# Kernel optimization log

Hardware: AMD Instinct MI355X
Metric: run time of the kernel (lower is better)

## Reference

```python
import jax, jax.numpy as jnp
import numpy as np
from math import comb

N, D, ORDER, P = 32768, 8, 19, 20
O = ORDER + 1


def bernstein(X, order):
    # X: [N, D] in [0,1] -> Bernstein basis [N, D, order+1]
    o = order + 1
    r = jnp.arange(o, dtype=X.dtype)
    binom = jnp.asarray([comb(order, k) for k in range(o)], dtype=X.dtype)
    Xe = X[..., None]
    return (Xe ** r) * ((1.0 - Xe) ** (order - r)) * binom


def setup_inputs() -> dict:
    key = jax.random.key(0)
    k0, k1, k2, k3, k4, k5 = jax.random.split(key, 6)
    X = jax.random.uniform(k0, (N, D), dtype=jnp.float32)
    # perm: each row is a permutation of range(D) (as in the module default)
    perm = jax.vmap(lambda k: jax.random.permutation(k, D))(jax.random.split(k1, P)).astype(jnp.int32)
    meanw0 = -0.2 + 0.1 * jax.random.normal(k2, (P, 1, O), dtype=jnp.float32)
    meanw = -0.2 + 0.1 * jax.random.normal(k3, (D - 1, P, O, O), dtype=jnp.float32)
    varw0 = 0.05 * jax.random.normal(k4, (P, 1, O), dtype=jnp.float32)
    varw = 0.05 * jax.random.normal(k5, (D - 1, P, O, O), dtype=jnp.float32)
    return {"X": X, "perm": perm, "meanw0": meanw0, "meanw": meanw,
            "varw0": varw0, "varw": varw}


def reference(X, perm, meanw0, meanw, varw0, varw):
    outB = bernstein(X, ORDER)                       # [N, D, O]
    outBp = jnp.transpose(outB[:, perm], (1, 0, 2, 3))  # gather axis=1 -> [P, N, D, O]

    # ---- f_mean: chain of small matmuls with exp(meanw_i), gated by basis ----
    f = jnp.exp(meanw0) * outBp[:, :, 0, :]          # [P,1,O]*[P,N,O] -> [P,N,O]
    for i in range(1, D):
        f = jnp.einsum('pno,poq->pnq', f, jnp.exp(meanw[i - 1])) * outBp[:, :, i, :]
    mean = jnp.sum(jnp.sum(f, axis=-1), axis=0)[:, None]   # [N,1]

    # ---- f_var: six moment chains one..six, exp(meanw)^2 * exp(varw)^k ----
    kk = jnp.arange(1, 7, dtype=X.dtype).reshape(6, 1, 1, 1)
    B2_0 = outBp[:, :, 0, :] ** 2                    # [P,N,O]
    acc = jnp.exp(2.0 * meanw0 + kk * varw0) * B2_0[None]  # [6,P,N,O]
    for i in range(1, D):
        Wi = jnp.exp(2.0 * meanw[i - 1] + kk * varw[i - 1])  # [6,P,O,O]
        acc = jnp.einsum('kpno,kpoq->kpnq', acc, Wi) * (outBp[:, :, i, :] ** 2)[None]
    mom = jnp.sum(acc, axis=-1)                      # [6,P,N]
    c = jnp.asarray([1.0, 1 / 2, 1 / 6, 1 / 24, 1 / 120, 1 / 720], dtype=X.dtype)
    var = jnp.einsum('k,kpn->n', c, mom)[:, None]    # [N,1]

    return jnp.concatenate([mean, var], axis=-1)     # [N,2]
```

## Files before the change

kernel.cpp:

```cpp
#include <hip/hip_runtime.h>
#include <math.h>

#define NPTS 32768
#define DD 8
#define OO 20
#define PP 20
#define NCHAIN 7
#define NT 2

typedef _Float16 half8 __attribute__((ext_vector_type(8)));
typedef __fp16 fp16x2 __attribute__((ext_vector_type(2)));
typedef float floatx16 __attribute__((ext_vector_type(16)));
typedef unsigned int u32;

#define AS1 __attribute__((address_space(1)))
#define AS3 __attribute__((address_space(3)))

__device__ __forceinline__ int sigma_row(int m) {
    return (m >= 4 && m < 12) ? (m ^ 12) : m;
}

__device__ __forceinline__ void basis20(float tv, float* g) {
    constexpr float binom[OO] = {
        1.f, 19.f, 171.f, 969.f, 3876.f, 11628.f, 27132.f, 50388.f, 75582.f,
        92378.f, 92378.f, 75582.f, 50388.f, 27132.f, 11628.f, 3876.f, 969.f,
        171.f, 19.f, 1.f};
    float a = tv, b = 1.f - tv, v = 1.f;
#pragma unroll
    for (int q = 0; q < OO; ++q) { g[q] = v; v *= a; }
    v = 1.f;
#pragma unroll
    for (int q = OO - 1; q >= 0; --q) { g[q] = g[q] * v * binom[q]; v *= b; }
}

__device__ __forceinline__ unsigned pk2rtn(float a, float b) {
    union { _Float16 h[2]; unsigned u; } cv;
    cv.h[0] = (_Float16)a; cv.h[1] = (_Float16)b;
    return cv.u;
}

__device__ __forceinline__ unsigned pack_pk(float x, float y) {
    union { fp16x2 h; unsigned u; } cv;
    cv.h = __builtin_amdgcn_cvt_pkrtz(x, y);
    return cv.u;
}

__device__ __forceinline__ fp16x2 u2h(unsigned u) {
    union { unsigned u; fp16x2 h; } c; c.u = u; return c.h;
}
__device__ __forceinline__ unsigned h2u(fp16x2 h) {
    union { unsigned u; fp16x2 h; } c; c.h = h; return c.u;
}

__global__ void prep_kernel(const float* __restrict__ X,
                            const float* __restrict__ meanw0,
                            const float* __restrict__ meanw,
                            const float* __restrict__ varw0,
                            const float* __restrict__ varw,
                            float* __restrict__ W0,
                            _Float16* __restrict__ WA,
                            unsigned* __restrict__ G) {
    int e = blockIdx.x * 256 + threadIdx.x;
    const int n0 = NCHAIN * PP * OO;
    const int nW = NCHAIN * (DD - 1) * PP * 32 * 32;
    const int nG = NPTS * DD;
    if (e < n0) {
        int q = e % OO;
        int rem = e / OO;
        int p = rem % PP;
        int c = rem / PP;
        float m = meanw0[p * OO + q];
        W0[e] = (c == 0) ? __expf(m) : __expf(2.f * m + (float)c * varw0[p * OO + q]);
    } else if (e < n0 + nW) {
        int idx = e - n0;
        int j = idx & 7; idx >>= 3;
        int l = idx & 63; idx >>= 6;
        int f = idx & 1; idx >>= 1;
        int p = idx % PP; idx /= PP;
        int i = idx % (DD - 1);
        int c = idx / (DD - 1);
        int m = l & 31;
        int k = (l >> 5) * 8 + f * 16 + j;
        int q = sigma_row(m);
        float v = 0.f;
        if (q < OO && k < OO) {
            int mi = ((i * PP + p) * OO + k) * OO + q;
            float mm = meanw[mi];
            v = (c == 0) ? __expf(mm) : __expf(2.f * mm + (float)c * varw[mi]);
        }
        WA[e - n0] = (_Float16)v;
    } else if (e < n0 + nW + nG) {
        int idx = e - n0 - nW;
        int n = idx & (NPTS - 1);
        int d = idx >> 15;
        float g[OO];
        basis20(X[(size_t)n * DD + d], g);
        uint4 o0, o1, o2;
        o0.x = pk2rtn(g[0], g[1]);
        o0.y = pk2rtn(g[2], g[3]);
        o0.z = pk2rtn(g[4], g[5]);
        o0.w = pk2rtn(g[6], g[7]);
        o1.x = pk2rtn(g[16], g[17]);
        o1.y = pk2rtn(g[18], g[19]);
        o1.z = pk2rtn(g[8], g[9]);
        o1.w = pk2rtn(g[10], g[11]);
        o2.x = pk2rtn(g[12], g[13]);
        o2.y = pk2rtn(g[14], g[15]);
        o2.z = 0u;
        o2.w = 0u;
        uint4* out = (uint4*)(G + (size_t)(d * NPTS + n) * 12);
        out[0] = o0; out[1] = o1; out[2] = o2;
    }
}

__global__ __launch_bounds__(256, 2) void chain_kernel(
    const int* __restrict__ perm,
    const float* __restrict__ W0, const _Float16* __restrict__ WA,
    const unsigned* __restrict__ G, float* __restrict__ partial) {
    const int lane = threadIdx.x & 63;
    const int wv = threadIdx.x >> 6;
    const int nl = lane & 31;
    const bool hi = (lane >> 5) != 0;
    const int n0 = (blockIdx.x * 4 + wv) * (32 * NT);
    const int p = blockIdx.y;
    const int goffd = hi ? 6 : 0;

    __shared__ __align__(16) _Float16 Alds[2][NCHAIN * 1024];

    int dp[DD];
#pragma unroll
    for (int i = 0; i < DD; ++i) dp[i] = perm[p * DD + i];

    const unsigned uz = ((unsigned)dp[0]) >> 20;
    const float fz = __uint_as_float(uz);
    floatx16 kZero;
#pragma unroll
    for (int r = 0; r < 16; ++r) kZero[r] = fz;

    {
        const _Float16* wbase = WA + (size_t)p * 1024;
#pragma unroll
        for (int u = wv; u < 2 * NCHAIN; u += 4) {
            int c = u >> 1, h = u & 1;
            const _Float16* src =
                wbase + (size_t)c * (DD - 1) * PP * 1024 + h * 512 + lane * 8;
            __builtin_amdgcn_global_load_lds(
                (const AS1 u32*)src, (AS3 u32*)&Alds[0][u * 512], 16, 0, 0);
        }
    }

    unsigned st[NT][NCHAIN][6];

#pragma unroll
    for (int tile = 0; tile < NT; ++tile) {
        const uint2* rp = (const uint2*)(
            G + ((size_t)dp[0] * NPTS + (n0 + tile * 32 + nl)) * 12 + goffd);
        uint2 r0 = rp[0], r1 = rp[1], r2 = rp[2];
        unsigned gw[6] = {r0.x, r0.y, r1.x, r1.y, r2.x, r2.y};
        float gcf[12], scf[12];
#pragma unroll
        for (int q = 0; q < 6; ++q) {
            fp16x2 gh = u2h(gw[q]);
            gcf[2 * q] = (float)gh.x; gcf[2 * q + 1] = (float)gh.y;
        }
#pragma unroll
        for (int r = 0; r < 12; ++r) scf[r] = gcf[r] * gcf[r];
#pragma unroll
        for (int c = 0; c < NCHAIN; ++c) {
            const float* w0r = W0 + (c * PP + p) * OO;
            float val[12];
#pragma unroll
            for (int r = 0; r < 8; ++r) {
                float ws = hi ? w0r[r + 8] : w0r[r];
                val[r] = ws * (c == 0 ? gcf[r] : scf[r]);
            }
#pragma unroll
            for (int r = 8; r < 12; ++r) {
                float ws = hi ? 0.f : w0r[r + 8];
                val[r] = ws * (c == 0 ? gcf[r] : scf[r]);
            }
#pragma unroll
            for (int e = 0; e < 6; ++e)
                st[tile][c][e] = pack_pk(val[2 * e], val[2 * e + 1]);
        }
    }

    const float coef[NCHAIN] = {0.f, 1.f, 0.5f, 1.f / 6.f, 1.f / 24.f,
                                1.f / 120.f, 1.f / 720.f};
    float sm[NT], sv[NT];
#pragma unroll
    for (int tile = 0; tile < NT; ++tile) { sm[tile] = 0.f; sv[tile] = 0.f; }

    __syncthreads();

#pragma unroll
    for (int i = 1; i < DD; ++i) {
        const int cur = (i - 1) & 1;

        if (i < DD - 1) {
            const _Float16* wbase = WA + (size_t)(i * PP + p) * 1024;
#pragma unroll
            for (int u = wv; u < 2 * NCHAIN; u += 4) {
                int c = u >> 1, h = u & 1;
                const _Float16* src =
                    wbase + (size_t)c * (DD - 1) * PP * 1024 + h * 512 + lane * 8;
                __builtin_amdgcn_global_load_lds(
                    (const AS1 u32*)src, (AS3 u32*)&Alds[cur ^ 1][u * 512], 16, 0, 0);
            }
        }

        unsigned gw[NT][6], sw[NT][6];
#pragma unroll
        for (int tile = 0; tile < NT; ++tile) {
            const uint2* rp = (const uint2*)(
                G + ((size_t)dp[i] * NPTS + (n0 + tile * 32 + nl)) * 12 + goffd);
            uint2 r0 = rp[0], r1 = rp[1], r2 = rp[2];
            gw[tile][0] = r0.x; gw[tile][1] = r0.y;
            gw[tile][2] = r1.x; gw[tile][3] = r1.y;
            gw[tile][4] = r2.x; gw[tile][5] = r2.y;
        }
        if (i < DD - 1) {
#pragma unroll
            for (int tile = 0; tile < NT; ++tile)
#pragma unroll
                for (int e = 0; e < 6; ++e) {
                    fp16x2 gh = u2h(gw[tile][e]);
                    sw[tile][e] = h2u(gh * gh);
                }
        }

        float gcf[NT][12], scf[NT][12];
        if (i == DD - 1) {
#pragma unroll
            for (int tile = 0; tile < NT; ++tile) {
#pragma unroll
                for (int q = 0; q < 6; ++q) {
                    fp16x2 gh = u2h(gw[tile][q]);
                    gcf[tile][2 * q] = (float)gh.x; gcf[tile][2 * q + 1] = (float)gh.y;
                }
#pragma unroll
                for (int r = 0; r < 12; ++r)
                    scf[tile][r] = gcf[tile][r] * gcf[tile][r];
            }
        }

#pragma unroll
        for (int c = 0; c < NCHAIN; ++c) {
            const _Float16* ab = &Alds[cur][c * 1024 + lane * 8];
            half8 A0 = *(const half8*)(ab);
            half8 A1 = *(const half8*)(ab + 512);

#pragma unroll
            for (int tile = 0; tile < NT; ++tile) {
                union { unsigned u[4]; half8 h; } B0, B1;
                B0.u[0] = st[tile][c][0]; B0.u[1] = st[tile][c][1];
                B0.u[2] = st[tile][c][2]; B0.u[3] = st[tile][c][3];
                B1.u[0] = st[tile][c][4]; B1.u[1] = st[tile][c][5];
                B1.u[2] = uz;             B1.u[3] = uz;

                floatx16 acc;
                acc = __builtin_amdgcn_mfma_f32_32x32x16_f16(A0, B0.h, kZero, 0, 0, 0);
                acc = __builtin_amdgcn_mfma_f32_32x32x16_f16(A1, B1.h, acc, 0, 0, 0);

                if (i < DD - 1) {
#pragma unroll
                    for (int e = 0; e < 6; ++e) {
                        fp16x2 pr = __builtin_amdgcn_cvt_pkrtz(acc[2 * e], acc[2 * e + 1]);
                        fp16x2 gv = u2h(c == 0 ? gw[tile][e] : sw[tile][e]);
                        st[tile][c][e] = h2u(pr * gv);
                    }
                } else {
                    float s = 0.f;
#pragma unroll
                    for (int r = 0; r < 12; ++r)
                        s += acc[r] * (c == 0 ? gcf[tile][r] : scf[tile][r]);
                    if (c == 0) sm[tile] = s;
                    else        sv[tile] += coef[c] * s;
                }
            }
        }

        if (i < DD - 1) __syncthreads();
    }

#pragma unroll
    for (int tile = 0; tile < NT; ++tile) {
        float m = sm[tile] + __shfl_xor(sm[tile], 32, 64);
        float v = sv[tile] + __shfl_xor(sv[tile], 32, 64);
        if (lane < 32) {
            partial[(size_t)p * NPTS + n0 + tile * 32 + nl] = m;
            partial[(size_t)(PP + p) * NPTS + n0 + tile * 32 + nl] = v;
        }
    }
}

__global__ void reduce_kernel(const float* __restrict__ partial,
                              float* __restrict__ out) {
    int n = blockIdx.x * 256 + threadIdx.x;
    float m = 0.f, v = 0.f;
#pragma unroll
    for (int p = 0; p < PP; ++p) {
        m += partial[(size_t)p * NPTS + n];
        v += partial[(size_t)(PP + p) * NPTS + n];
    }
    out[2 * n] = m;
    out[2 * n + 1] = v;
}

extern "C" void kernel_launch(void* const* d_in, const int* in_sizes, int n_in,
                              void* d_out, int out_size, void* d_ws, size_t ws_size,
                              hipStream_t stream) {
    const float* X      = (const float*)d_in[0];
    const int*   perm   = (const int*)d_in[1];
    const float* meanw0 = (const float*)d_in[2];
    const float* meanw  = (const float*)d_in[3];
    const float* varw0  = (const float*)d_in[4];
    const float* varw   = (const float*)d_in[5];
    float* out = (float*)d_out;

    float*     W0      = (float*)d_ws;
    _Float16*  WA      = (_Float16*)((char*)d_ws + 11200);
    unsigned*  G       = (unsigned*)((char*)d_ws + 11200 + 2007040);
    float*     partial = (float*)((char*)d_ws + 11200 + 2007040 + 12582912);

    int prep_n = NCHAIN * PP * OO + NCHAIN * (DD - 1) * PP * 32 * 32 + NPTS * DD;
    hipLaunchKernelGGL(prep_kernel, dim3((prep_n + 255) / 256), dim3(256), 0,
                       stream, X, meanw0, meanw, varw0, varw, W0, WA, G);

    dim3 grid(NPTS / (128 * NT), PP);
    hipLaunchKernelGGL(chain_kernel, grid, dim3(256), 0, stream,
                       perm, W0, WA, G, partial);

    hipLaunchKernelGGL(reduce_kernel, dim3(NPTS / 256), dim3(256), 0, stream,
                       partial, out);
}
```

Measured before the change: 145.2 us.

## Fuse final reduction into chain kernel via atomic counter; shrink basis stride

The separate reduce kernel is replaced by a last-block-done pattern: each chain block bumps a per-column atomic counter and the block that finishes last sums the P partials and writes the output. This removes one kernel launch and its dependency gap. The basis table G is also packed at 10 words per point instead of 12, dropping the zero padding, and the padded lanes are filled with zero in registers. This cuts G storage and load traffic, at the cost of a fence, an atomic and a serialized reduction tail inside the chain kernel.

```diff
diff --git a/kernel.cpp b/kernel.cpp
--- a/kernel.cpp
+++ b/kernel.cpp
@@ -7,6 +7,7 @@
 #define PP 20
 #define NCHAIN 7
 #define NT 2
+#define GSTRIDE 10
 
 typedef _Float16 half8 __attribute__((ext_vector_type(8)));
 typedef __fp16 fp16x2 __attribute__((ext_vector_type(2)));
@@ -59,7 +60,8 @@
                             const float* __restrict__ varw,
                             float* __restrict__ W0,
                             _Float16* __restrict__ WA,
-                            unsigned* __restrict__ G) {
+                            unsigned* __restrict__ G,
+                            unsigned* __restrict__ cnt) {
     int e = blockIdx.x * 256 + threadIdx.x;
     const int n0 = NCHAIN * PP * OO;
     const int nW = NCHAIN * (DD - 1) * PP * 32 * 32;
@@ -95,28 +97,29 @@
         int d = idx >> 15;
         float g[OO];
         basis20(X[(size_t)n * DD + d], g);
-        uint4 o0, o1, o2;
+        uint2 o0, o1, o2, o3, o4;
         o0.x = pk2rtn(g[0], g[1]);
         o0.y = pk2rtn(g[2], g[3]);
-        o0.z = pk2rtn(g[4], g[5]);
-        o0.w = pk2rtn(g[6], g[7]);
-        o1.x = pk2rtn(g[16], g[17]);
-        o1.y = pk2rtn(g[18], g[19]);
-        o1.z = pk2rtn(g[8], g[9]);
-        o1.w = pk2rtn(g[10], g[11]);
-        o2.x = pk2rtn(g[12], g[13]);
-        o2.y = pk2rtn(g[14], g[15]);
-        o2.z = 0u;
-        o2.w = 0u;
-        uint4* out = (uint4*)(G + (size_t)(d * NPTS + n) * 12);
-        out[0] = o0; out[1] = o1; out[2] = o2;
+        o1.x = pk2rtn(g[4], g[5]);
+        o1.y = pk2rtn(g[6], g[7]);
+        o2.x = pk2rtn(g[16], g[17]);
+        o2.y = pk2rtn(g[18], g[19]);
+        o3.x = pk2rtn(g[8], g[9]);
+        o3.y = pk2rtn(g[10], g[11]);
+        o4.x = pk2rtn(g[12], g[13]);
+        o4.y = pk2rtn(g[14], g[15]);
+        uint2* out = (uint2*)(G + (size_t)(d * NPTS + n) * GSTRIDE);
+        out[0] = o0; out[1] = o1; out[2] = o2; out[3] = o3; out[4] = o4;
+    } else if (e < n0 + nW + nG + 128) {
+        cnt[e - n0 - nW - nG] = 0u;
     }
 }
 
 __global__ __launch_bounds__(256, 2) void chain_kernel(
     const int* __restrict__ perm,
     const float* __restrict__ W0, const _Float16* __restrict__ WA,
-    const unsigned* __restrict__ G, float* __restrict__ partial) {
+    const unsigned* __restrict__ G, float* __restrict__ partial,
+    unsigned* __restrict__ cnt, float* __restrict__ out) {
     const int lane = threadIdx.x & 63;
     const int wv = threadIdx.x >> 6;
     const int nl = lane & 31;
@@ -126,6 +129,7 @@
     const int goffd = hi ? 6 : 0;
 
     __shared__ __align__(16) _Float16 Alds[2][NCHAIN * 1024];
+    __shared__ bool isLast;
 
     int dp[DD];
 #pragma unroll
@@ -154,9 +158,10 @@
 #pragma unroll
     for (int tile = 0; tile < NT; ++tile) {
         const uint2* rp = (const uint2*)(
-            G + ((size_t)dp[0] * NPTS + (n0 + tile * 32 + nl)) * 12 + goffd);
+            G + ((size_t)dp[0] * NPTS + (n0 + tile * 32 + nl)) * GSTRIDE + goffd);
         uint2 r0 = rp[0], r1 = rp[1], r2 = rp[2];
-        unsigned gw[6] = {r0.x, r0.y, r1.x, r1.y, r2.x, r2.y};
+        unsigned gw[6] = {r0.x, r0.y, r1.x, r1.y,
+                          hi ? uz : r2.x, hi ? uz : r2.y};
         float gcf[12], scf[12];
 #pragma unroll
         for (int q = 0; q < 6; ++q) {
@@ -213,11 +218,11 @@
 #pragma unroll
         for (int tile = 0; tile < NT; ++tile) {
             const uint2* rp = (const uint2*)(
-                G + ((size_t)dp[i] * NPTS + (n0 + tile * 32 + nl)) * 12 + goffd);
+                G + ((size_t)dp[i] * NPTS + (n0 + tile * 32 + nl)) * GSTRIDE + goffd);
             uint2 r0 = rp[0], r1 = rp[1], r2 = rp[2];
             gw[tile][0] = r0.x; gw[tile][1] = r0.y;
             gw[tile][2] = r1.x; gw[tile][3] = r1.y;
-            gw[tile][4] = r2.x; gw[tile][5] = r2.y;
+            gw[tile][4] = hi ? uz : r2.x; gw[tile][5] = hi ? uz : r2.y;
         }
         if (i < DD - 1) {
 #pragma unroll
@@ -292,19 +297,26 @@
             partial[(size_t)(PP + p) * NPTS + n0 + tile * 32 + nl] = v;
         }
     }
-}
-
-__global__ void reduce_kernel(const float* __restrict__ partial,
-                              float* __restrict__ out) {
-    int n = blockIdx.x * 256 + threadIdx.x;
-    float m = 0.f, v = 0.f;
-#pragma unroll
-    for (int p = 0; p < PP; ++p) {
-        m += partial[(size_t)p * NPTS + n];
-        v += partial[(size_t)(PP + p) * NPTS + n];
-    }
-    out[2 * n] = m;
-    out[2 * n + 1] = v;
+
+    __syncthreads();
+    if (threadIdx.x == 0) {
+        __threadfence();
+        unsigned old = atomicAdd(&cnt[blockIdx.x], 1u);
+        isLast = (old == PP - 1);
+    }
+    __syncthreads();
+    if (isLast) {
+        __threadfence();
+        int n = blockIdx.x * 256 + threadIdx.x;
+        float m = 0.f, v = 0.f;
+#pragma unroll
+        for (int p2 = 0; p2 < PP; ++p2) {
+            m += partial[(size_t)p2 * NPTS + n];
+            v += partial[(size_t)(PP + p2) * NPTS + n];
+        }
+        out[2 * n] = m;
+        out[2 * n + 1] = v;
+    }
 }
 
 extern "C" void kernel_launch(void* const* d_in, const int* in_sizes, int n_in,
@@ -321,16 +333,15 @@
     float*     W0      = (float*)d_ws;
     _Float16*  WA      = (_Float16*)((char*)d_ws + 11200);
     unsigned*  G       = (unsigned*)((char*)d_ws + 11200 + 2007040);
-    float*     partial = (float*)((char*)d_ws + 11200 + 2007040 + 12582912);
-
-    int prep_n = NCHAIN * PP * OO + NCHAIN * (DD - 1) * PP * 32 * 32 + NPTS * DD;
+    float*     partial = (float*)((char*)d_ws + 11200 + 2007040 + 10485760);
+    unsigned*  cnt     = (unsigned*)((char*)d_ws + 11200 + 2007040 + 10485760 + 5242880);
+
+    int prep_n = NCHAIN * PP * OO + NCHAIN * (DD - 1) * PP * 32 * 32
+               + NPTS * DD + 128;
     hipLaunchKernelGGL(prep_kernel, dim3((prep_n + 255) / 256), dim3(256), 0,
-                       stream, X, meanw0, meanw, varw0, varw, W0, WA, G);
+                       stream, X, meanw0, meanw, varw0, varw, W0, WA, G, cnt);
 
     dim3 grid(NPTS / (128 * NT), PP);
     hipLaunchKernelGGL(chain_kernel, grid, dim3(256), 0, stream,
-                       perm, W0, WA, G, partial);
-
-    hipLaunchKernelGGL(reduce_kernel, dim3(NPTS / 256), dim3(256), 0, stream,
-                       partial, out);
-}
+                       perm, W0, WA, G, partial, cnt, out);
+}
```

Result: slower. 206.1 us (+41.9%).
